# Kernel optimization log

Hardware: AMD Instinct MI355X
Metric: run time of the kernel (lower is better)

## Reference

```python
import jax, jax.numpy as jnp
import numpy as np
from jax import lax

K = 9
CENTER = K // 2
EXTEND = 1.0
EPS = 1e-5
GROUPS = 16  # out_ch // 4


def conv2d(x, w, b, stride, padding):
    y = lax.conv_general_dilated(x, w, window_strides=stride, padding=padding,
                                 dimension_numbers=('NCHW', 'OIHW', 'NCHW'))
    return y + b[None, :, None, None]


def setup_inputs() -> dict:
    key = jax.random.key(0)
    ks = jax.random.split(key, 9)
    B, C, Wd, Hd, OUT = 8, 64, 128, 128, 64
    f = jax.random.normal(ks[0], (B, C, Wd, Hd), jnp.float32)
    w_off = jax.random.normal(ks[1], (2 * K, C, 3, 3), jnp.float32) * 0.05
    b_off = jax.random.normal(ks[2], (2 * K,), jnp.float32) * 0.05
    bn_gamma = 1.0 + 0.1 * jax.random.normal(ks[3], (2 * K,), jnp.float32)
    bn_beta = 0.1 * jax.random.normal(ks[4], (2 * K,), jnp.float32)
    w_dsc = jax.random.normal(ks[5], (OUT, C, K, 1), jnp.float32) * 0.05
    b_dsc = jax.random.normal(ks[6], (OUT,), jnp.float32) * 0.05
    gn_gamma = 1.0 + 0.1 * jax.random.normal(ks[7], (OUT,), jnp.float32)
    gn_beta = 0.1 * jax.random.normal(ks[8], (OUT,), jnp.float32)
    return {'f': f, 'w_off': w_off, 'b_off': b_off, 'bn_gamma': bn_gamma,
            'bn_beta': bn_beta, 'w_dsc': w_dsc, 'b_dsc': b_dsc,
            'gn_gamma': gn_gamma, 'gn_beta': gn_beta}


def _forward(f, w_off, b_off, bn_gamma, bn_beta, w_dsc, b_dsc, gn_gamma, gn_beta):
    B, C, Wd, Hd = f.shape  # module names: width=shape[2], height=shape[3]
    dt = f.dtype

    # offset branch: conv3x3 -> BatchNorm (training mode, batch stats) -> tanh
    off = conv2d(f, w_off, b_off, (1, 1), 'SAME')
    mu = off.mean(axis=(0, 2, 3), keepdims=True)
    var = off.var(axis=(0, 2, 3), keepdims=True)
    off = (off - mu) / jnp.sqrt(var + EPS)
    off = off * bn_gamma[None, :, None, None] + bn_beta[None, :, None, None]
    off = jnp.tanh(off)

    y_off = off[:, :K]  # [B,K,Wd,Hd]; x_off (off[:, K:]) unused for morph=0

    # cumulative offset scan from the center point (morph=0).
    # NOTE: endpoints 0 and K-1 keep detached raw offsets (torch detach().clone()).
    raw0 = lax.stop_gradient(y_off)
    offn = [None] * K
    offn[CENTER] = jnp.zeros_like(y_off[:, 0])
    for i in range(1, CENTER):
        offn[CENTER + i] = offn[CENTER + i - 1] + y_off[:, CENTER + i]
        offn[CENTER - i] = offn[CENTER - i + 1] + y_off[:, CENTER - i]
    offn[0] = raw0[:, 0]
    offn[K - 1] = raw0[:, K - 1]
    offn = jnp.stack(offn, axis=1)  # [B,K,Wd,Hd]

    # coordinate grids: y indexes the width axis, x the height axis
    y_new = jnp.arange(Wd, dtype=dt)[None, None, :, None] + offn * EXTEND  # [B,K,Wd,Hd]
    x_new = ((jnp.arange(K, dtype=dt) - CENTER)[None, :, None, None]
             + jnp.arange(Hd, dtype=dt)[None, None, None, :])  # [1,K,1,Hd]
    x_new = jnp.broadcast_to(x_new, (B, K, Wd, Hd))

    # layout [B, K*Wd, Hd] via (B,K,Wd,Hd) -> (B,Wd,K,Hd)
    y_s = jnp.transpose(y_new, (0, 2, 1, 3)).reshape(B, K * Wd * Hd)
    x_s = jnp.transpose(x_new, (0, 2, 1, 3)).reshape(B, K * Wd * Hd)

    # bilinear interpolation (clamped corner indices, unclamped y/x in weights)
    y0 = jnp.floor(y_s).astype(jnp.int32)
    x0 = jnp.floor(x_s).astype(jnp.int32)
    y0c = jnp.clip(y0, 0, Wd - 1)
    y1c = jnp.clip(y0 + 1, 0, Wd - 1)
    x0c = jnp.clip(x0, 0, Hd - 1)
    x1c = jnp.clip(x0 + 1, 0, Hd - 1)

    feat = jnp.transpose(f, (0, 2, 3, 1)).reshape(B, Wd * Hd, C)

    def gather(yi, xi):
        idx = (yi * Hd + xi)[:, :, None]  # [B,N,1]
        return jnp.take_along_axis(feat, idx, axis=1)  # [B,N,C]

    va0 = gather(y0c, x0c)
    vc0 = gather(y0c, x1c)
    va1 = gather(y1c, x0c)
    vc1 = gather(y1c, x1c)

    y0f, y1f = y0c.astype(dt), y1c.astype(dt)
    x0f, x1f = x0c.astype(dt), x1c.astype(dt)
    wa = ((y1f - y_s) * (x1f - x_s))[:, :, None]
    wb = ((y1f - y_s) * (x_s - x0f))[:, :, None]
    wc = ((y_s - y0f) * (x1f - x_s))[:, :, None]
    wd = ((y_s - y0f) * (x_s - x0f))[:, :, None]

    out = va0 * wa + vc0 * wb + va1 * wc + vc1 * wd  # [B,N,C]
    deformed = jnp.transpose(out.reshape(B, K * Wd, Hd, C), (0, 3, 1, 2))  # [B,C,K*Wd,Hd]

    # strided conv over the K snake points -> [B,OUT,Wd,Hd]
    x = conv2d(deformed, w_dsc, b_dsc, (K, 1), 'VALID')

    # GroupNorm + ReLU
    OUT = x.shape[1]
    xg = x.reshape(B, GROUPS, -1)
    gmu = xg.mean(axis=-1, keepdims=True)
    gvar = xg.var(axis=-1, keepdims=True)
    xg = (xg - gmu) / jnp.sqrt(gvar + EPS)
    x = xg.reshape(x.shape) * gn_gamma[None, :, None, None] + gn_beta[None, :, None, None]
    return jax.nn.relu(x)


def reference(f, w_off, b_off, bn_gamma, bn_beta, w_dsc, b_dsc, gn_gamma, gn_beta):
    return _forward(f, w_off, b_off, bn_gamma, bn_beta, w_dsc, b_dsc, gn_gamma, gn_beta)
```

## Files before the change

kernel.cpp:

```cpp
#include <hip/hip_runtime.h>

#define B_   8
#define C_   64
#define W_   128
#define H_   128
#define K_   9
#define OUT_ 64
#define NPIX (B_*W_*H_)
#define EPS_ 1e-5f

typedef __attribute__((ext_vector_type(8))) short bf16x8;
typedef __attribute__((ext_vector_type(4))) float f32x4;

#define FEATBF_OFF  0
#define XPRE_OFF    4194304
#define OFFPRE_OFF  12582912
#define WT_OFF      13762560
#define WP_OFF      13780992
#define BNSTATS_OFF 13786176
#define BNAB_OFF    13786194
#define GSTATS_OFF  13786212
#define GNFIN_OFF   13786468
#define STATS_BYTES ((18+18+256+256)*sizeof(float))

__device__ __forceinline__ unsigned pack2bf(float a, float b) {
    union { float f; unsigned u; } ua, ub;
    ua.f = a; ub.f = b;
    unsigned x = ua.u, y = ub.u;
    x += 0x7fffu + ((x >> 16) & 1u);
    y += 0x7fffu + ((y >> 16) & 1u);
    return (x >> 16) | (y & 0xffff0000u);
}
__device__ __forceinline__ float bflo(unsigned u) {
    union { unsigned u; float f; } v; v.u = u << 16; return v.f;
}
__device__ __forceinline__ float bfhi(unsigned u) {
    union { unsigned u; float f; } v; v.u = u & 0xffff0000u; return v.f;
}

__global__ __launch_bounds__(256) void k_nhwc(const float* __restrict__ f,
                                              unsigned short* __restrict__ featbf) {
    __shared__ float tile[64][65];
    int bid = blockIdx.x;
    int ht = bid & 1;
    int w  = (bid >> 1) & 127;
    int b  = bid >> 8;
    int t  = threadIdx.x;
    int lh = t & 63;
    int c0 = (t >> 6) * 16;
    const float* fp = f + (((b*64)*128 + w)*128) + ht*64 + lh;
#pragma unroll
    for (int i = 0; i < 16; i++) {
        int c = c0 + i;
        tile[c][lh] = fp[c*16384];
    }
    __syncthreads();
    int lc = t & 63;
    int h0 = (t >> 6) * 16;
    unsigned short* obf = featbf + ((size_t)((b*128 + w)*128) + ht*64)*64 + lc;
#pragma unroll
    for (int i = 0; i < 16; i++) {
        int hr = h0 + i;
        union { float f; unsigned u; } v; v.f = tile[lc][hr];
        unsigned x = v.u + 0x7fffu + ((v.u >> 16) & 1u);
        obf[(size_t)hr*64] = (unsigned short)(x >> 16);
    }
}

__global__ void k_wt(const float* __restrict__ w_dsc, unsigned short* __restrict__ wTbf) {
    int i = blockIdx.x*256 + threadIdx.x;
    if (i >= 9*64*64) return;
    int c = i & 63;
    int o = (i >> 6) & 63;
    int k = i >> 12;
    union { float f; unsigned u; } v;
    v.f = w_dsc[(o*64 + c)*9 + k];
    unsigned x = v.u + 0x7fffu + ((v.u >> 16) & 1u);
    wTbf[i] = (unsigned short)(x >> 16);
}

__global__ void k_wp(const float* __restrict__ w_off, float* __restrict__ wP) {
    int i = blockIdx.x*256 + threadIdx.x;
    if (i >= 64*81) return;
    int c    = i / 81;
    int rem  = i % 81;
    int dw   = rem / 27;
    int rem2 = rem % 27;
    int ck   = rem2 / 3;
    int dh   = rem2 % 3;
    wP[i] = w_off[ck*576 + c*9 + dw*3 + dh];
}

__global__ __launch_bounds__(128) void k_conv_off(const float* __restrict__ f,
                                                  const float* __restrict__ wP,
                                                  const float* __restrict__ b_off,
                                                  float* __restrict__ off_pre,
                                                  float* __restrict__ bnstats) {
    __shared__ float wred[2][18];
    int t   = threadIdx.x;
    int bid = blockIdx.x;
    int b   = bid & 7;
    int w   = bid >> 3;
    int h   = t;

    float em = (h == 0)   ? 0.f : 1.f;
    float ep = (h == 127) ? 0.f : 1.f;
    int   om = h + ((h == 0)   ? 0 : -1);
    int   op = h + ((h == 127) ? 0 : 1);

    const float* fb = f + (size_t)b*1048576 + (size_t)w*128;

    float acc[9];
#pragma unroll
    for (int ck = 0; ck < 9; ck++) acc[ck] = b_off[ck];

#pragma unroll 2
    for (int c = 0; c < 64; c++) {
        const float* p  = fb + c*16384;
        const float* wc = wP + c*81;
#pragma unroll
        for (int dw = -1; dw <= 1; dw++) {
            int wy = w + dw;
            if ((unsigned)wy < 128u) {
                const float* q = p + dw*128;
                float v0 = q[om] * em;
                float v1 = q[h];
                float v2 = q[op] * ep;
                const float* ww = wc + (dw+1)*27;
#pragma unroll
                for (int ck = 0; ck < 9; ck++)
                    acc[ck] += v0*ww[ck*3] + v1*ww[ck*3+1] + v2*ww[ck*3+2];
            }
        }
    }

    int pixoff = (w << 7) + h;
#pragma unroll
    for (int ck = 0; ck < 9; ck++)
        off_pre[((b*9 + ck) << 14) + pixoff] = acc[ck];

    float s[9], q[9];
#pragma unroll
    for (int ck = 0; ck < 9; ck++) { s[ck] = acc[ck]; q[ck] = acc[ck]*acc[ck]; }
    for (int off = 32; off; off >>= 1) {
#pragma unroll
        for (int ck = 0; ck < 9; ck++) {
            s[ck] += __shfl_down(s[ck], off);
            q[ck] += __shfl_down(q[ck], off);
        }
    }
    int wid = t >> 6;
    if ((t & 63) == 0) {
#pragma unroll
        for (int ck = 0; ck < 9; ck++) {
            wred[wid][ck]   = s[ck];
            wred[wid][9+ck] = q[ck];
        }
    }
    __syncthreads();
    if (t < 18) {
        float v = wred[0][t] + wred[1][t];
        int ck  = (t < 9) ? t : t-9;
        atomicAdd(&bnstats[ck*2 + (t < 9 ? 0 : 1)], v);
    }
}

__global__ void k_bn_fin(const float* __restrict__ bnstats,
                         const float* __restrict__ bn_gamma,
                         const float* __restrict__ bn_beta,
                         float* __restrict__ bnAB) {
    int t = threadIdx.x;
    if (t < 9) {
        float n    = (float)NPIX;
        float mean = bnstats[t*2] / n;
        float var  = bnstats[t*2+1] / n - mean*mean;
        float A    = bn_gamma[t] / sqrtf(var + EPS_);
        bnAB[t*2]   = A;
        bnAB[t*2+1] = bn_beta[t] - mean * A;
    }
}

__global__ __launch_bounds__(256) void k_sample_dsc(const unsigned short* __restrict__ featbf,
                                                    const float* __restrict__ off_pre,
                                                    const float* __restrict__ bnAB,
                                                    const unsigned short* __restrict__ wTbf,
                                                    const float* __restrict__ b_dsc,
                                                    float* __restrict__ xpre,
                                                    float* __restrict__ gstats) {
    __shared__ __align__(16) unsigned char lds_samp[128*128];
    __shared__ __align__(16) unsigned char lds_wk[64*128];
    __shared__ float ynew[9][128];
    __shared__ float red[16][2];

    int t = threadIdx.x;
    int b = blockIdx.x & 7, w = blockIdx.x >> 3;

    if (t < 128) {
        int h = t;
        float y[9];
#pragma unroll
        for (int ck = 0; ck < 9; ck++) {
            float v = off_pre[((b*9+ck) << 14) + (w << 7) + h];
            y[ck] = tanhf(bnAB[ck*2]*v + bnAB[ck*2+1]);
        }
        float ofn[9];
        ofn[4] = 0.f;
        ofn[5] = y[5]; ofn[6] = y[5]+y[6]; ofn[7] = y[5]+y[6]+y[7];
        ofn[3] = y[3]; ofn[2] = y[3]+y[2]; ofn[1] = y[3]+y[2]+y[1];
        ofn[0] = y[0]; ofn[8] = y[8];
#pragma unroll
        for (int k = 0; k < 9; k++) ynew[k][h] = (float)w + ofn[k];
    }
    if (t < 16) { red[t][0] = 0.f; red[t][1] = 0.f; }

    f32x4 acc[2][4];
#pragma unroll
    for (int mi = 0; mi < 2; mi++)
#pragma unroll
        for (int ni = 0; ni < 4; ni++) {
            acc[mi][ni][0] = 0.f; acc[mi][ni][1] = 0.f;
            acc[mi][ni][2] = 0.f; acc[mi][ni][3] = 0.f;
        }

    int lane = t & 63, wv = t >> 6;
    int m0 = wv * 32;
    int lm = lane & 15, lk = lane >> 4;
    int hs = t >> 1;
    int cq = (t & 1) * 4;

    __syncthreads();

    for (int k = 0; k < 9; k++) {
        if (k) __syncthreads();

        {
            const uint4* src = (const uint4*)(wTbf + (k << 12));
#pragma unroll
            for (int i = 0; i < 2; i++) {
                int ci = t + i*256;
                uint4 v = src[ci];
                int o  = ci >> 3;
                int cb = (ci & 7) << 4;
                *(uint4*)(lds_wk + o*128 + (cb ^ ((o & 7) << 4))) = v;
            }
        }

        {
            int x0 = k - 4 + hs;
            unsigned char* dst = lds_samp + hs*128;
            int bcol0 = (t & 1) * 64;
            if ((unsigned)x0 < 127u) {
                float ys = ynew[k][hs];
                int y0  = (int)floorf(ys);
                int y0c = min(max(y0, 0), 127), y1c = min(max(y0+1, 0), 127);
                float wa = (float)y1c - ys;
                float wc = ys - (float)y0c;
                const unsigned short* pb = featbf + ((size_t)b << 20);
                const uint4* p0 = (const uint4*)(pb + (y0c*128 + x0)*64) + cq;
                const uint4* p1 = (const uint4*)(pb + (y1c*128 + x0)*64) + cq;
#pragma unroll
                for (int ci = 0; ci < 4; ci++) {
                    uint4 a = p0[ci], c = p1[ci];
                    uint4 u;
                    u.x = pack2bf(bflo(a.x)*wa + bflo(c.x)*wc, bfhi(a.x)*wa + bfhi(c.x)*wc);
                    u.y = pack2bf(bflo(a.y)*wa + bflo(c.y)*wc, bfhi(a.y)*wa + bfhi(c.y)*wc);
                    u.z = pack2bf(bflo(a.z)*wa + bflo(c.z)*wc, bfhi(a.z)*wa + bfhi(c.z)*wc);
                    u.w = pack2bf(bflo(a.w)*wa + bflo(c.w)*wc, bfhi(a.w)*wa + bfhi(c.w)*wc);
                    *(uint4*)(dst + ((bcol0 + ci*16) ^ ((hs & 7) << 4))) = u;
                }
            } else {
                uint4 z = make_uint4(0,0,0,0);
#pragma unroll
                for (int ci = 0; ci < 4; ci++)
                    *(uint4*)(dst + ((bcol0 + ci*16) ^ ((hs & 7) << 4))) = z;
            }
        }
        __syncthreads();

#pragma unroll
        for (int ks = 0; ks < 2; ks++) {
            bf16x8 af[2], bfr[4];
#pragma unroll
            for (int mi = 0; mi < 2; mi++) {
                int h = m0 + mi*16 + lm;
                af[mi] = *(const bf16x8*)(lds_samp + h*128 + ((ks*64 + lk*16) ^ ((h & 7) << 4)));
            }
#pragma unroll
            for (int ni = 0; ni < 4; ni++) {
                int o = ni*16 + lm;
                bfr[ni] = *(const bf16x8*)(lds_wk + o*128 + ((ks*64 + lk*16) ^ ((o & 7) << 4)));
            }
#pragma unroll
            for (int mi = 0; mi < 2; mi++)
#pragma unroll
                for (int ni = 0; ni < 4; ni++)
                    acc[mi][ni] = __builtin_amdgcn_mfma_f32_16x16x32_bf16(af[mi], bfr[ni], acc[mi][ni], 0, 0, 0);
        }
    }

#pragma unroll
    for (int ni = 0; ni < 4; ni++) {
        int o = ni*16 + lm;
        float bias = b_dsc[o];
        float s1 = 0.f, s2 = 0.f;
#pragma unroll
        for (int mi = 0; mi < 2; mi++) {
            float4 r;
            r.x = acc[mi][ni][0] + bias;
            r.y = acc[mi][ni][1] + bias;
            r.z = acc[mi][ni][2] + bias;
            r.w = acc[mi][ni][3] + bias;
            s1 += r.x + r.y + r.z + r.w;
            s2 += r.x*r.x + r.y*r.y + r.z*r.z + r.w*r.w;
            int h = m0 + mi*16 + lk*4;
            *(float4*)(xpre + (((b*64 + o) << 14) + (w << 7) + h)) = r;
        }
        s1 += __shfl_xor(s1, 1);  s1 += __shfl_xor(s1, 2);
        s1 += __shfl_xor(s1, 16); s1 += __shfl_xor(s1, 32);
        s2 += __shfl_xor(s2, 1);  s2 += __shfl_xor(s2, 2);
        s2 += __shfl_xor(s2, 16); s2 += __shfl_xor(s2, 32);
        if (lk == 0 && (lm & 3) == 0) {
            atomicAdd(&red[ni*4 + (lm >> 2)][0], s1);
            atomicAdd(&red[ni*4 + (lm >> 2)][1], s2);
        }
    }
    __syncthreads();
    if (t < 16) {
        atomicAdd(&gstats[(b*16 + t)*2],   red[t][0]);
        atomicAdd(&gstats[(b*16 + t)*2+1], red[t][1]);
    }
}

__global__ void k_gn_fin(const float* __restrict__ gstats, float* __restrict__ gnfin) {
    int t = threadIdx.x;
    if (t < 128) {
        float n    = 65536.f;
        float mean = gstats[t*2] / n;
        float var  = gstats[t*2+1] / n - mean*mean;
        gnfin[t*2]   = mean;
        gnfin[t*2+1] = 1.0f / sqrtf(var + EPS_);
    }
}

__global__ __launch_bounds__(256) void k_gn_apply(const float* __restrict__ xpre,
                                                  const float* __restrict__ gnfin,
                                                  const float* __restrict__ gn_gamma,
                                                  const float* __restrict__ gn_beta,
                                                  float* __restrict__ out) {
    int i4  = blockIdx.x*256 + threadIdx.x;
    int idx = i4 * 4;
    int o = (idx >> 14) & 63;
    int b = idx >> 20;
    int g = o >> 2;
    float mean = gnfin[(b*16+g)*2];
    float istd = gnfin[(b*16+g)*2+1];
    float ga = gn_gamma[o] * istd;
    float be = gn_beta[o] - mean * ga;
    float4 v = *(const float4*)(xpre + idx);
    v.x = fmaxf(v.x*ga + be, 0.f);
    v.y = fmaxf(v.y*ga + be, 0.f);
    v.z = fmaxf(v.z*ga + be, 0.f);
    v.w = fmaxf(v.w*ga + be, 0.f);
    *(float4*)(out + idx) = v;
}

extern "C" void kernel_launch(void* const* d_in, const int* in_sizes, int n_in,
                              void* d_out, int out_size, void* d_ws, size_t ws_size,
                              hipStream_t stream) {
    const float* f        = (const float*)d_in[0];
    const float* w_off    = (const float*)d_in[1];
    const float* b_off    = (const float*)d_in[2];
    const float* bn_gamma = (const float*)d_in[3];
    const float* bn_beta  = (const float*)d_in[4];
    const float* w_dsc    = (const float*)d_in[5];
    const float* b_dsc    = (const float*)d_in[6];
    const float* gn_gamma = (const float*)d_in[7];
    const float* gn_beta  = (const float*)d_in[8];

    float* ws      = (float*)d_ws;
    unsigned short* featbf = (unsigned short*)(ws + FEATBF_OFF);
    float* xpre    = ws + XPRE_OFF;
    float* off_pre = ws + OFFPRE_OFF;
    unsigned short* wTbf = (unsigned short*)(ws + WT_OFF);
    float* wP      = ws + WP_OFF;
    float* bnstats = ws + BNSTATS_OFF;
    float* bnAB    = ws + BNAB_OFF;
    float* gstats  = ws + GSTATS_OFF;
    float* gnfin   = ws + GNFIN_OFF;

    hipMemsetAsync(bnstats, 0, STATS_BYTES, stream);

    k_nhwc<<<2048, 256, 0, stream>>>(f, featbf);
    k_wt<<<144, 256, 0, stream>>>(w_dsc, wTbf);
    k_wp<<<21, 256, 0, stream>>>(w_off, wP);
    k_conv_off<<<1024, 128, 0, stream>>>(f, wP, b_off, off_pre, bnstats);
    k_bn_fin<<<1, 32, 0, stream>>>(bnstats, bn_gamma, bn_beta, bnAB);
    k_sample_dsc<<<1024, 256, 0, stream>>>(featbf, off_pre, bnAB, wTbf, b_dsc, xpre, gstats);
    k_gn_fin<<<1, 128, 0, stream>>>(gstats, gnfin);
    k_gn_apply<<<8192, 256, 0, stream>>>(xpre, gnfin, gn_gamma, gn_beta, (float*)d_out);
}
```

Measured before the change: 138.3 us.

## Split offset conv over channel halves and move BN stats into a reduce kernel

The 3x3 offset convolution now runs with twice as many blocks, each summing over half of the input channels and writing a partial result. A new kernel adds the two partials, writes the offset pre-activations and accumulates the BatchNorm sums. The conv bias is dropped because training-mode BatchNorm subtracts the per-channel mean, which cancels any constant bias. This aims to raise occupancy on the conv stage. In exchange it adds an extra launch and an extra round trip of partial buffers through global memory.

```diff
diff --git a/kernel.cpp b/kernel.cpp
--- a/kernel.cpp
+++ b/kernel.cpp
@@ -15,12 +15,13 @@
 #define FEATBF_OFF  0
 #define XPRE_OFF    4194304
 #define OFFPRE_OFF  12582912
-#define WT_OFF      13762560
-#define WP_OFF      13780992
-#define BNSTATS_OFF 13786176
-#define BNAB_OFF    13786194
-#define GSTATS_OFF  13786212
-#define GNFIN_OFF   13786468
+#define OFFH_OFF    13762560
+#define WT_OFF      16121856
+#define WP_OFF      16140288
+#define BNSTATS_OFF 16145472
+#define BNAB_OFF    16145490
+#define GSTATS_OFF  16145508
+#define GNFIN_OFF   16145764
 #define STATS_BYTES ((18+18+256+256)*sizeof(float))
 
 __device__ __forceinline__ unsigned pack2bf(float a, float b) {
@@ -93,14 +94,12 @@
 
 __global__ __launch_bounds__(128) void k_conv_off(const float* __restrict__ f,
                                                   const float* __restrict__ wP,
-                                                  const float* __restrict__ b_off,
-                                                  float* __restrict__ off_pre,
-                                                  float* __restrict__ bnstats) {
-    __shared__ float wred[2][18];
+                                                  float* __restrict__ off_half) {
     int t   = threadIdx.x;
     int bid = blockIdx.x;
     int b   = bid & 7;
-    int w   = bid >> 3;
+    int w   = (bid >> 3) & 127;
+    int ch  = bid >> 10;
     int h   = t;
 
     float em = (h == 0)   ? 0.f : 1.f;
@@ -108,16 +107,17 @@
     int   om = h + ((h == 0)   ? 0 : -1);
     int   op = h + ((h == 127) ? 0 : 1);
 
-    const float* fb = f + (size_t)b*1048576 + (size_t)w*128;
+    const float* fb = f + (size_t)b*1048576 + (size_t)(ch*32)*16384 + (size_t)w*128;
+    const float* wb = wP + ch*32*81;
 
     float acc[9];
 #pragma unroll
-    for (int ck = 0; ck < 9; ck++) acc[ck] = b_off[ck];
-
-#pragma unroll 2
-    for (int c = 0; c < 64; c++) {
+    for (int ck = 0; ck < 9; ck++) acc[ck] = 0.f;
+
+#pragma unroll 4
+    for (int c = 0; c < 32; c++) {
         const float* p  = fb + c*16384;
-        const float* wc = wP + c*81;
+        const float* wc = wb + c*81;
 #pragma unroll
         for (int dw = -1; dw <= 1; dw++) {
             int wy = w + dw;
@@ -134,35 +134,48 @@
         }
     }
 
+    float* dst = off_half + (size_t)ch*1179648;
     int pixoff = (w << 7) + h;
 #pragma unroll
     for (int ck = 0; ck < 9; ck++)
-        off_pre[((b*9 + ck) << 14) + pixoff] = acc[ck];
-
-    float s[9], q[9];
-#pragma unroll
-    for (int ck = 0; ck < 9; ck++) { s[ck] = acc[ck]; q[ck] = acc[ck]*acc[ck]; }
+        dst[((b*9 + ck) << 14) + pixoff] = acc[ck];
+}
+
+__global__ __launch_bounds__(256) void k_bn_stats(const float* __restrict__ off_half,
+                                                  float* __restrict__ off_pre,
+                                                  float* __restrict__ bnstats) {
+    __shared__ float wred[4][2];
+    int bid = blockIdx.x;
+    int b  = bid / 36;
+    int rem = bid % 36;
+    int ck = rem / 4;
+    int wq = rem % 4;
+    int t  = threadIdx.x;
+    int base4 = (((b*9+ck) << 14) + wq*4096) >> 2;
+
+    const float4* h0 = (const float4*)off_half;
+    const float4* h1 = (const float4*)(off_half + 1179648);
+    float4* op = (float4*)off_pre;
+
+    float s = 0.f, q = 0.f;
+#pragma unroll
+    for (int i = 0; i < 4; i++) {
+        int idx = base4 + t + i*256;
+        float4 a = h0[idx], bb = h1[idx];
+        float4 v;
+        v.x = a.x + bb.x; v.y = a.y + bb.y; v.z = a.z + bb.z; v.w = a.w + bb.w;
+        op[idx] = v;
+        s += v.x + v.y + v.z + v.w;
+        q += v.x*v.x + v.y*v.y + v.z*v.z + v.w*v.w;
+    }
     for (int off = 32; off; off >>= 1) {
-#pragma unroll
-        for (int ck = 0; ck < 9; ck++) {
-            s[ck] += __shfl_down(s[ck], off);
-            q[ck] += __shfl_down(q[ck], off);
-        }
-    }
-    int wid = t >> 6;
-    if ((t & 63) == 0) {
-#pragma unroll
-        for (int ck = 0; ck < 9; ck++) {
-            wred[wid][ck]   = s[ck];
-            wred[wid][9+ck] = q[ck];
-        }
-    }
+        s += __shfl_down(s, off);
+        q += __shfl_down(q, off);
+    }
+    if ((t & 63) == 0) { wred[t >> 6][0] = s; wred[t >> 6][1] = q; }
     __syncthreads();
-    if (t < 18) {
-        float v = wred[0][t] + wred[1][t];
-        int ck  = (t < 9) ? t : t-9;
-        atomicAdd(&bnstats[ck*2 + (t < 9 ? 0 : 1)], v);
-    }
+    if (t == 0) atomicAdd(&bnstats[ck*2],   wred[0][0]+wred[1][0]+wred[2][0]+wred[3][0]);
+    if (t == 1) atomicAdd(&bnstats[ck*2+1], wred[0][1]+wred[1][1]+wred[2][1]+wred[3][1]);
 }
 
 __global__ void k_bn_fin(const float* __restrict__ bnstats,
@@ -369,7 +382,6 @@
                               hipStream_t stream) {
     const float* f        = (const float*)d_in[0];
     const float* w_off    = (const float*)d_in[1];
-    const float* b_off    = (const float*)d_in[2];
     const float* bn_gamma = (const float*)d_in[3];
     const float* bn_beta  = (const float*)d_in[4];
     const float* w_dsc    = (const float*)d_in[5];
@@ -381,6 +393,7 @@
     unsigned short* featbf = (unsigned short*)(ws + FEATBF_OFF);
     float* xpre    = ws + XPRE_OFF;
     float* off_pre = ws + OFFPRE_OFF;
+    float* off_half= ws + OFFH_OFF;
     unsigned short* wTbf = (unsigned short*)(ws + WT_OFF);
     float* wP      = ws + WP_OFF;
     float* bnstats = ws + BNSTATS_OFF;
@@ -393,7 +406,8 @@
     k_nhwc<<<2048, 256, 0, stream>>>(f, featbf);
     k_wt<<<144, 256, 0, stream>>>(w_dsc, wTbf);
     k_wp<<<21, 256, 0, stream>>>(w_off, wP);
-    k_conv_off<<<1024, 128, 0, stream>>>(f, wP, b_off, off_pre, bnstats);
+    k_conv_off<<<2048, 128, 0, stream>>>(f, wP, off_half);
+    k_bn_stats<<<288, 256, 0, stream>>>(off_half, off_pre, bnstats);
     k_bn_fin<<<1, 32, 0, stream>>>(bnstats, bn_gamma, bn_beta, bnAB);
     k_sample_dsc<<<1024, 256, 0, stream>>>(featbf, off_pre, bnAB, wTbf, b_dsc, xpre, gstats);
     k_gn_fin<<<1, 128, 0, stream>>>(gstats, gnfin);
```

Result: faster. 124.1 us (-10.2%).
